# Kernel optimization log

Hardware: AMD Instinct MI355X
Metric: run time of the kernel (lower is better)

The kernel has to match this reference:

```python
import jax, jax.numpy as jnp
import numpy as np

RGB_W = (0.2989, 0.587, 0.114)
EPS = 1e-8  # guard only; original divides without eps


def _saliency_map(img):
    """Faithful jax port of SaliencyMap: gray -> uint8 -> cv2.Sobel(ksize=3,
    BORDER_REFLECT_101) -> magnitude -> per-image min-max normalize.
    img: [B, C, H, W] float in [0,1]. Returns [B, 1, H, W] float32.
    """
    B, C, H, W = img.shape
    if C == 3:
        gray = RGB_W[0] * img[:, 0] + RGB_W[1] * img[:, 1] + RGB_W[2] * img[:, 2]
    else:
        gray = img[:, 0]
    # (gray*255).astype(np.uint8): truncating cast, then cv2 promotes to float
    q = (gray * 255.0).astype(jnp.uint8).astype(jnp.float32)  # [B,H,W]
    # cv2 default border: BORDER_REFLECT_101 == jnp.pad mode 'reflect'
    p = jnp.pad(q, ((0, 0), (1, 1), (1, 1)), mode='reflect')  # [B,H+2,W+2]
    # Sobel x (correlation with [[-1,0,1],[-2,0,2],[-1,0,1]])
    gx = (p[:, :-2, 2:] + 2.0 * p[:, 1:-1, 2:] + p[:, 2:, 2:]
          - p[:, :-2, :-2] - 2.0 * p[:, 1:-1, :-2] - p[:, 2:, :-2])
    # Sobel y (transpose kernel)
    gy = (p[:, 2:, :-2] + 2.0 * p[:, 2:, 1:-1] + p[:, 2:, 2:]
          - p[:, :-2, :-2] - 2.0 * p[:, :-2, 1:-1] - p[:, :-2, 2:])
    mag = jnp.sqrt(gx * gx + gy * gy)  # [B,H,W]
    mn = jnp.min(mag, axis=(1, 2), keepdims=True)
    mx = jnp.max(mag, axis=(1, 2), keepdims=True)
    norm = (mag - mn) / jnp.maximum(mx - mn, EPS)  # cv2 NORM_MINMAX to [0,1]
    return norm[:, None]  # [B,1,H,W]


def setup_inputs() -> dict:
    key = jax.random.key(0)
    k1, k2, k3 = jax.random.split(key, 3)
    shape = (16, 3, 512, 512)
    return {
        "img_vis": jax.random.uniform(k1, shape, dtype=jnp.float32),
        "img_ir": jax.random.uniform(k2, shape, dtype=jnp.float32),
        "img_fusion": jax.random.uniform(k3, shape, dtype=jnp.float32),
    }


def reference(img_vis, img_ir, img_fusion):
    s_vis = _saliency_map(img_vis)  # [B,1,H,W]
    s_ir = _saliency_map(img_ir)
    denom = s_vis + s_ir + EPS  # eps guard against 0/0 (see notes)
    w_vis = s_vis / denom
    w_ir = s_ir / denom
    img_sal = w_vis * img_vis + w_ir * img_ir  # broadcasts over channels
    loss = jnp.mean(jnp.abs(img_sal - img_fusion))  # F.l1_loss (mean)
    return loss
```

## Files before the change

kernel.cpp:

```cpp
#include <hip/hip_runtime.h>
#include <hip/hip_bf16.h>
#include <stdint.h>

#define H 512
#define W 512
#define HW (H * W)
#define TR 8
#define NSTRIP (H / TR)
#define NSLOT (TR + 2)
#define LSTR 520

__device__ __forceinline__ int refl(int i, int n) {
    return i < 0 ? -i : (i >= n ? 2 * n - 2 - i : i);
}

__device__ __forceinline__ void cols10(uint2 lo, uint2 hi, float* __restrict__ c) {
    c[0] = (float)(lo.x >> 24);
    c[1] = (float)(lo.y & 0xffu);
    c[2] = (float)((lo.y >> 8) & 0xffu);
    c[3] = (float)((lo.y >> 16) & 0xffu);
    c[4] = (float)(lo.y >> 24);
    c[5] = (float)(hi.x & 0xffu);
    c[6] = (float)((hi.x >> 8) & 0xffu);
    c[7] = (float)((hi.x >> 16) & 0xffu);
    c[8] = (float)(hi.x >> 24);
    c[9] = (float)(hi.y & 0xffu);
}

__global__ __launch_bounds__(256) void k_sal(const float* __restrict__ vis,
                                             const float* __restrict__ ir,
                                             uint8_t* __restrict__ qvis,
                                             uint8_t* __restrict__ qir,
                                             float* __restrict__ pm, int B) {
    __shared__ uint8_t g[NSLOT][LSTR];
    __shared__ float red[4][2];
    int tid = threadIdx.x;
    int per_src = B * NSTRIP;
    int blk = blockIdx.x;
    int src = blk >= per_src;
    int rem = src ? blk - per_src : blk;
    int b     = rem >> 6;
    int strip = rem & 63;
    int y0 = strip * TR;

    const float4* p4 = (const float4*)((src ? ir : vis) + (size_t)b * 3 * HW);
    uint8_t* q = (src ? qir : qvis) + (size_t)b * HW;

    float4 Rc, Gc, Bc, Rn, Gn, Bn;
    {
        int t = tid, j = t >> 7, seg = t & 127;
        int row = refl(y0 - 1 + j, H);
        int o = row * (W / 4) + seg;
        Rc = p4[o];
        Gc = p4[o + HW / 4];
        Bc = p4[o + 2 * (HW / 4)];
    }
    #pragma unroll
    for (int it = 0; it < 5; ++it) {
        if (it < 4) {
            int t = tid + (it + 1) * 256, j = t >> 7, seg = t & 127;
            int row = refl(y0 - 1 + j, H);
            int o = row * (W / 4) + seg;
            Rn = p4[o];
            Gn = p4[o + HW / 4];
            Bn = p4[o + 2 * (HW / 4)];
        }
        __builtin_amdgcn_sched_barrier(0);
        {
            int t = tid + it * 256, j = t >> 7, seg = t & 127;
            uchar4 qq;
            qq.x = (uint8_t)((0.2989f * Rc.x + 0.587f * Gc.x + 0.114f * Bc.x) * 255.0f);
            qq.y = (uint8_t)((0.2989f * Rc.y + 0.587f * Gc.y + 0.114f * Bc.y) * 255.0f);
            qq.z = (uint8_t)((0.2989f * Rc.z + 0.587f * Gc.z + 0.114f * Bc.z) * 255.0f);
            qq.w = (uint8_t)((0.2989f * Rc.w + 0.587f * Gc.w + 0.114f * Bc.w) * 255.0f);
            *(uchar4*)&g[j][4 + seg * 4] = qq;
        }
        Rc = Rn; Gc = Gn; Bc = Bn;
    }
    __syncthreads();
    if (tid < NSLOT) {
        g[tid][3]   = g[tid][5];
        g[tid][516] = g[tid][514];
    }
    __syncthreads();

    float mn = INFINITY, mx = 0.0f;
    #pragma unroll
    for (int k = 0; k < 2; ++k) {
        int task = tid + k * 256;
        int r  = task >> 6;
        int s8 = task & 63;
        const uint8_t* rp0 = &g[r][s8 * 8];
        const uint8_t* rp1 = &g[r + 1][s8 * 8];
        const uint8_t* rp2 = &g[r + 2][s8 * 8];
        uint2 a0 = *(const uint2*)rp0, b0 = *(const uint2*)(rp0 + 8);
        uint2 a1 = *(const uint2*)rp1, b1 = *(const uint2*)(rp1 + 8);
        uint2 a2 = *(const uint2*)rp2, b2 = *(const uint2*)(rp2 + 8);
        uint2 qw; qw.x = a1.y; qw.y = b1.x;
        *(uint2*)(q + (size_t)(y0 + r) * W + s8 * 8) = qw;
        float c0[10], c1[10], c2[10];
        cols10(a0, b0, c0);
        cols10(a1, b1, c1);
        cols10(a2, b2, c2);
        float sx[10], sy[10];
        #pragma unroll
        for (int j = 0; j < 10; ++j) {
            sx[j] = c0[j] + 2.0f * c1[j] + c2[j];
            sy[j] = c2[j] - c0[j];
        }
        #pragma unroll
        for (int p = 0; p < 8; ++p) {
            float gx = sx[p + 2] - sx[p];
            float gy = sy[p] + 2.0f * sy[p + 1] + sy[p + 2];
            float m = sqrtf(gx * gx + gy * gy);
            mn = fminf(mn, m);
            mx = fmaxf(mx, m);
        }
    }

    #pragma unroll
    for (int o = 32; o > 0; o >>= 1) {
        mn = fminf(mn, __shfl_down(mn, o));
        mx = fmaxf(mx, __shfl_down(mx, o));
    }
    int lane = tid & 63, w = tid >> 6;
    if (lane == 0) { red[w][0] = mn; red[w][1] = mx; }
    __syncthreads();
    if (tid == 0) {
        #pragma unroll
        for (int ww = 1; ww < 4; ++ww) {
            mn = fminf(mn, red[ww][0]);
            mx = fmaxf(mx, red[ww][1]);
        }
        float* o = pm + ((size_t)(src * B + b) * NSTRIP + strip) * 2;
        o[0] = mn;
        o[1] = mx;
    }
}

__device__ __forceinline__ void row_cols(uint2 v, int lane, float* __restrict__ c) {
    uint32_t lx = __shfl_up(v.y, 1);
    uint32_t rx = __shfl_down(v.x, 1);
    uint32_t lb = (lane == 0)  ? ((v.x >> 8) & 0xffu)  : (lx >> 24);
    uint32_t rb = (lane == 63) ? ((v.y >> 16) & 0xffu) : (rx & 0xffu);
    c[0] = (float)lb;
    c[1] = (float)(v.x & 0xffu);
    c[2] = (float)((v.x >> 8) & 0xffu);
    c[3] = (float)((v.x >> 16) & 0xffu);
    c[4] = (float)(v.x >> 24);
    c[5] = (float)(v.y & 0xffu);
    c[6] = (float)((v.y >> 8) & 0xffu);
    c[7] = (float)((v.y >> 16) & 0xffu);
    c[8] = (float)(v.y >> 24);
    c[9] = (float)rb;
}

__device__ __forceinline__ void sobel_row8(const uint8_t* __restrict__ q, int y, int lane,
                                           float* __restrict__ mag) {
    const uint2* rm = (const uint2*)(q + (size_t)refl(y - 1, H) * W);
    const uint2* r0 = (const uint2*)(q + (size_t)y * W);
    const uint2* rp = (const uint2*)(q + (size_t)refl(y + 1, H) * W);
    uint2 vm = rm[lane], v0 = r0[lane], vp = rp[lane];
    float c0[10], c1[10], c2[10];
    row_cols(vm, lane, c0);
    row_cols(v0, lane, c1);
    row_cols(vp, lane, c2);
    float sx[10], sy[10];
    #pragma unroll
    for (int j = 0; j < 10; ++j) {
        sx[j] = c0[j] + 2.0f * c1[j] + c2[j];
        sy[j] = c2[j] - c0[j];
    }
    #pragma unroll
    for (int k = 0; k < 8; ++k) {
        float gx = sx[k + 2] - sx[k];
        float gy = sy[k] + 2.0f * sy[k + 1] + sy[k + 2];
        mag[k] = sqrtf(gx * gx + gy * gy);
    }
}

__global__ __launch_bounds__(256) void k_loss(const float* __restrict__ vis,
                                              const float* __restrict__ ir,
                                              const float* __restrict__ fus,
                                              const uint8_t* __restrict__ qvis,
                                              const uint8_t* __restrict__ qir,
                                              const float* __restrict__ pm,
                                              float* __restrict__ partial, int B) {
    int w = threadIdx.x >> 6, lane = threadIdx.x & 63;
    int b = blockIdx.x >> 6;
    int y0 = (blockIdx.x & 63) * 8;

    __shared__ float sred[4];
    {
        int src = w >> 1, qsel = w & 1;
        float v = pm[((size_t)(src * B + b) * NSTRIP + lane) * 2 + qsel];
        if (qsel == 0) {
            #pragma unroll
            for (int o = 32; o > 0; o >>= 1) v = fminf(v, __shfl_down(v, o));
        } else {
            #pragma unroll
            for (int o = 32; o > 0; o >>= 1) v = fmaxf(v, __shfl_down(v, o));
        }
        if (lane == 0) sred[w] = v;
    }
    __syncthreads();
    float mn_v = sred[0], mx_v = sred[1], mn_i = sred[2], mx_i = sred[3];
    float inv_v = 1.0f / fmaxf(mx_v - mn_v, 1e-8f);
    float inv_i = 1.0f / fmaxf(mx_i - mn_i, 1e-8f);

    float acc = 0.0f;
    #pragma unroll
    for (int rr = 0; rr < 2; ++rr) {
        int y = y0 + w + rr * 4;
        float mv[8], mi[8];
        sobel_row8(qvis + (size_t)b * HW, y, lane, mv);
        sobel_row8(qir  + (size_t)b * HW, y, lane, mi);

        float wv[8], wi[8];
        #pragma unroll
        for (int k = 0; k < 8; ++k) {
            float sv = (mv[k] - mn_v) * inv_v;
            float si = (mi[k] - mn_i) * inv_i;
            float den = sv + si + 1e-8f;
            float rden = 1.0f / den;
            wv[k] = sv * rden;
            wi[k] = si * rden;
        }

        int i = y * W + lane * 8;
        #pragma unroll
        for (int ch = 0; ch < 3; ++ch) {
            size_t e4 = ((((size_t)b * 3 + ch) * HW) + i) >> 2;
            const float4* v4 = (const float4*)vis;
            const float4* r4 = (const float4*)ir;
            const float4* f4 = (const float4*)fus;
            float4 va = v4[e4], vb = v4[e4 + 1];
            float4 ra = r4[e4], rb = r4[e4 + 1];
            float4 fa = f4[e4], fb = f4[e4 + 1];
            acc += fabsf(wv[0] * va.x + wi[0] * ra.x - fa.x);
            acc += fabsf(wv[1] * va.y + wi[1] * ra.y - fa.y);
            acc += fabsf(wv[2] * va.z + wi[2] * ra.z - fa.z);
            acc += fabsf(wv[3] * va.w + wi[3] * ra.w - fa.w);
            acc += fabsf(wv[4] * vb.x + wi[4] * rb.x - fb.x);
            acc += fabsf(wv[5] * vb.y + wi[5] * rb.y - fb.y);
            acc += fabsf(wv[6] * vb.z + wi[6] * rb.z - fb.z);
            acc += fabsf(wv[7] * vb.w + wi[7] * rb.w - fb.w);
        }
    }

    #pragma unroll
    for (int o = 32; o > 0; o >>= 1) acc += __shfl_down(acc, o);
    __shared__ float ssum[4];
    if (lane == 0) ssum[w] = acc;
    __syncthreads();
    if (threadIdx.x == 0) partial[blockIdx.x] = ssum[0] + ssum[1] + ssum[2] + ssum[3];
}

__global__ void k_final(const float* __restrict__ partial, int n, float* __restrict__ out,
                        long long N) {
    double s = 0.0;
    for (int i = threadIdx.x; i < n; i += 256) s += (double)partial[i];
    __shared__ double sm[256];
    sm[threadIdx.x] = s;
    __syncthreads();
    for (int k = 128; k > 0; k >>= 1) {
        if (threadIdx.x < k) sm[threadIdx.x] += sm[threadIdx.x + k];
        __syncthreads();
    }
    if (threadIdx.x == 0) out[0] = (float)(sm[0] / (double)N);
}

extern "C" void kernel_launch(void* const* d_in, const int* in_sizes, int n_in,
                              void* d_out, int out_size, void* d_ws, size_t ws_size,
                              hipStream_t stream) {
    const float* vis = (const float*)d_in[0];
    const float* ir  = (const float*)d_in[1];
    const float* fus = (const float*)d_in[2];
    int B = in_sizes[0] / (3 * HW);

    uint8_t* qvis = (uint8_t*)d_ws;
    uint8_t* qir  = qvis + (size_t)B * HW;
    float* pm      = (float*)(qir + (size_t)B * HW);
    float* partial = pm + (size_t)2 * B * NSTRIP * 2;
    float* out = (float*)d_out;

    int nblk_sal = 2 * B * NSTRIP;
    k_sal<<<nblk_sal, 256, 0, stream>>>(vis, ir, qvis, qir, pm, B);

    int nblk_loss = B * (H / 8);
    k_loss<<<nblk_loss, 256, 0, stream>>>(vis, ir, fus, qvis, qir, pm, partial, B);

    k_final<<<1, 256, 0, stream>>>(partial, nblk_loss, out, (long long)B * 3 * HW);
}
```

Baseline: 56.39 us.

## Double saliency strip height and fuse final reduction into loss kernel via last-block atomic

Doubles the rows processed per saliency block, which halves the block count and reduces the fraction of halo rows reloaded. It also removes the separate final-reduction kernel: each loss block publishes its partial sum with release semantics and bumps an atomic counter, and the last block to arrive sums all partials. This saves one kernel launch but adds a memset launch and atomic traffic. The per-image min/max gather in the loss kernel now indexes only 32 strips, using lane&31, so each value is read twice, which is harmless for min and max.

Result: slower. 115.6 us (+105.0%).

```diff
diff --git a/kernel.cpp b/kernel.cpp
--- a/kernel.cpp
+++ b/kernel.cpp
@@ -5,7 +5,7 @@
 #define H 512
 #define W 512
 #define HW (H * W)
-#define TR 8
+#define TR 16
 #define NSTRIP (H / TR)
 #define NSLOT (TR + 2)
 #define LSTR 520
@@ -39,8 +39,8 @@
     int blk = blockIdx.x;
     int src = blk >= per_src;
     int rem = src ? blk - per_src : blk;
-    int b     = rem >> 6;
-    int strip = rem & 63;
+    int b     = rem >> 5;
+    int strip = rem & 31;
     int y0 = strip * TR;
 
     const float4* p4 = (const float4*)((src ? ir : vis) + (size_t)b * 3 * HW);
@@ -56,8 +56,8 @@
         Bc = p4[o + 2 * (HW / 4)];
     }
     #pragma unroll
-    for (int it = 0; it < 5; ++it) {
-        if (it < 4) {
+    for (int it = 0; it < 9; ++it) {
+        if (it < 8) {
             int t = tid + (it + 1) * 256, j = t >> 7, seg = t & 127;
             int row = refl(y0 - 1 + j, H);
             int o = row * (W / 4) + seg;
@@ -86,7 +86,7 @@
 
     float mn = INFINITY, mx = 0.0f;
     #pragma unroll
-    for (int k = 0; k < 2; ++k) {
+    for (int k = 0; k < 4; ++k) {
         int task = tid + k * 256;
         int r  = task >> 6;
         int s8 = task & 63;
@@ -185,7 +185,10 @@
                                               const uint8_t* __restrict__ qvis,
                                               const uint8_t* __restrict__ qir,
                                               const float* __restrict__ pm,
-                                              float* __restrict__ partial, int B) {
+                                              float* __restrict__ partial,
+                                              uint32_t* __restrict__ counter,
+                                              float* __restrict__ out,
+                                              int B, int nblk, long long N) {
     int w = threadIdx.x >> 6, lane = threadIdx.x & 63;
     int b = blockIdx.x >> 6;
     int y0 = (blockIdx.x & 63) * 8;
@@ -193,7 +196,7 @@
     __shared__ float sred[4];
     {
         int src = w >> 1, qsel = w & 1;
-        float v = pm[((size_t)(src * B + b) * NSTRIP + lane) * 2 + qsel];
+        float v = pm[((size_t)(src * B + b) * NSTRIP + (lane & 31)) * 2 + qsel];
         if (qsel == 0) {
             #pragma unroll
             for (int o = 32; o > 0; o >>= 1) v = fminf(v, __shfl_down(v, o));
@@ -251,23 +254,34 @@
     #pragma unroll
     for (int o = 32; o > 0; o >>= 1) acc += __shfl_down(acc, o);
     __shared__ float ssum[4];
+    __shared__ int is_last;
     if (lane == 0) ssum[w] = acc;
     __syncthreads();
-    if (threadIdx.x == 0) partial[blockIdx.x] = ssum[0] + ssum[1] + ssum[2] + ssum[3];
-}
-
-__global__ void k_final(const float* __restrict__ partial, int n, float* __restrict__ out,
-                        long long N) {
-    double s = 0.0;
-    for (int i = threadIdx.x; i < n; i += 256) s += (double)partial[i];
-    __shared__ double sm[256];
-    sm[threadIdx.x] = s;
-    __syncthreads();
-    for (int k = 128; k > 0; k >>= 1) {
-        if (threadIdx.x < k) sm[threadIdx.x] += sm[threadIdx.x + k];
+    if (threadIdx.x == 0) {
+        float blocksum = ssum[0] + ssum[1] + ssum[2] + ssum[3];
+        __hip_atomic_store(&partial[blockIdx.x], blocksum,
+                           __ATOMIC_RELEASE, __HIP_MEMORY_SCOPE_AGENT);
+        uint32_t old = __hip_atomic_fetch_add(counter, 1u,
+                           __ATOMIC_ACQ_REL, __HIP_MEMORY_SCOPE_AGENT);
+        is_last = (old == (uint32_t)(nblk - 1));
+    }
+    __syncthreads();
+    if (is_last) {
+        double s = 0.0;
+        for (int i = threadIdx.x; i < nblk; i += 256) {
+            float p = __hip_atomic_load(&partial[i],
+                         __ATOMIC_ACQUIRE, __HIP_MEMORY_SCOPE_AGENT);
+            s += (double)p;
+        }
+        __shared__ double sm[256];
+        sm[threadIdx.x] = s;
         __syncthreads();
-    }
-    if (threadIdx.x == 0) out[0] = (float)(sm[0] / (double)N);
+        for (int k = 128; k > 0; k >>= 1) {
+            if (threadIdx.x < k) sm[threadIdx.x] += sm[threadIdx.x + k];
+            __syncthreads();
+        }
+        if (threadIdx.x == 0) out[0] = (float)(sm[0] / (double)N);
+    }
 }
 
 extern "C" void kernel_launch(void* const* d_in, const int* in_sizes, int n_in,
@@ -282,13 +296,16 @@
     uint8_t* qir  = qvis + (size_t)B * HW;
     float* pm      = (float*)(qir + (size_t)B * HW);
     float* partial = pm + (size_t)2 * B * NSTRIP * 2;
+    uint32_t* counter = (uint32_t*)(partial + 1024);
     float* out = (float*)d_out;
+
+    hipMemsetAsync(counter, 0, sizeof(uint32_t), stream);
 
     int nblk_sal = 2 * B * NSTRIP;
     k_sal<<<nblk_sal, 256, 0, stream>>>(vis, ir, qvis, qir, pm, B);
 
     int nblk_loss = B * (H / 8);
-    k_loss<<<nblk_loss, 256, 0, stream>>>(vis, ir, fus, qvis, qir, pm, partial, B);
-
-    k_final<<<1, 256, 0, stream>>>(partial, nblk_loss, out, (long long)B * 3 * HW);
-}
+    k_loss<<<nblk_loss, 256, 0, stream>>>(vis, ir, fus, qvis, qir, pm, partial,
+                                          counter, out, B, nblk_loss,
+                                          (long long)B * 3 * HW);
+}
```
